# Optimization experiments

Measured on AMD Instinct MI355X. Metric: run time of the kernel, lower is better.

## Reference

```python
import jax, jax.numpy as jnp
import numpy as np

NEG_INF = -9e15
ALPHA = 2.0  # LeakyReLU negative slope from init (alpha=2)


def setup_inputs() -> dict:
    key = jax.random.key(0)
    k1, k2, k3, k4 = jax.random.split(key, 4)
    B, N, Fin, Fout = 8, 2048, 256, 128
    x = jax.random.normal(k1, (B, N, Fin), dtype=jnp.float32)
    adj = jax.random.randint(k2, (B, N, N), 0, 2, dtype=jnp.int32)
    # xavier_uniform with gain=1.414
    def xavier(k, shape, gain=1.414):
        fan_in, fan_out = shape[0], shape[1]
        bound = gain * np.sqrt(6.0 / (fan_in + fan_out))
        return jax.random.uniform(k, shape, jnp.float32, -bound, bound)
    W = xavier(k3, (Fin, Fout))
    a = xavier(k4, (2 * Fout, 1))
    return {"x": x, "adj": adj, "W": W, "a": a}


def reference(x, adj, W, a):
    # Wh: [B, N, Fout]
    Wh = jnp.matmul(x, W)
    Fout = W.shape[1]
    a1 = a[:Fout, 0]   # [Fout]
    a2 = a[Fout:, 0]   # [Fout]
    f1 = jnp.einsum('bnf,f->bn', Wh, a1)  # [B, N]
    f2 = jnp.einsum('bnf,f->bn', Wh, a2)  # [B, N]
    e = f1[:, :, None] + f2[:, None, :]   # [B, N, N]
    e = jnp.where(e >= 0, e, ALPHA * e)   # leaky relu, slope 2
    e = jnp.where(adj > 0, e, NEG_INF)
    attention = jax.nn.softmax(e, axis=2)
    # dropout: eval mode (no-op)
    h_prime = jnp.matmul(attention, Wh)   # [B, N, Fout]
    # concat=True -> elu
    return jnp.where(h_prime > 0, h_prime, jnp.expm1(h_prime))
```

## Files before the change

kernel.cpp:

```cpp
#include <hip/hip_runtime.h>
#include <hip/hip_bf16.h>
#include <math.h>

constexpr int B_   = 8;
constexpr int N_   = 2048;
constexpr int FIN  = 256;
constexpr int FOUT = 128;

constexpr int CH  = 512;
constexpr int NCH = N_ / CH;
constexpr int PR  = CH + 8;
constexpr int XR  = FIN + 8;
constexpr int TR  = 40;

typedef __attribute__((ext_vector_type(8))) short bf16x8;
typedef __attribute__((ext_vector_type(4))) float f32x4;
typedef __attribute__((ext_vector_type(4))) int   i32x4;

static __device__ __forceinline__ unsigned short f2bf(float f) {
    __hip_bfloat16 h = __float2bfloat16(f);
    return *reinterpret_cast<unsigned short*>(&h);
}
static __device__ __forceinline__ i32x4 ntload4(const int* p) {
    return __builtin_nontemporal_load((const i32x4*)p);
}

__global__ __launch_bounds__(256) void k0_wt(const float* __restrict__ W,
                                             unsigned short* __restrict__ Wt) {
    const int n = blockIdx.x;
    const int k = threadIdx.x;
    Wt[n * FIN + k] = f2bf(W[k * FOUT + n]);
}

__global__ __launch_bounds__(256) void ka_wh(const float* __restrict__ x,
                                             const unsigned short* __restrict__ Wt,
                                             const float* __restrict__ a,
                                             unsigned short* __restrict__ WhT,
                                             float* __restrict__ f1,
                                             float* __restrict__ f2) {
    __shared__ unsigned short xs[32 * XR];
    __shared__ float as[2 * FOUT];
    __shared__ float fred[2][4][32];

    const int tid = threadIdx.x;
    const int j0  = blockIdx.x * 32;
    const int b   = j0 >> 11;
    const int jb  = j0 & (N_ - 1);

    if (tid < 2 * FOUT) as[tid] = a[tid];
    {
        const float4* xsrc = (const float4*)(x + (size_t)j0 * FIN);
#pragma unroll
        for (int t = 0; t < 8; ++t) {
            const int idx = tid + t * 256;
            float4 v = xsrc[idx];
            const int row = idx >> 6, c4 = idx & 63;
            ushort4 u;
            u.x = f2bf(v.x); u.y = f2bf(v.y); u.z = f2bf(v.z); u.w = f2bf(v.w);
            *(ushort4*)&xs[row * XR + c4 * 4] = u;
        }
    }
    __syncthreads();

    const int wave = tid >> 6, lane = tid & 63;
    const int quad = lane >> 4, l16 = lane & 15;

    f32x4 acc[2][2];
#pragma unroll
    for (int aa = 0; aa < 2; ++aa)
#pragma unroll
        for (int nn = 0; nn < 2; ++nn) acc[aa][nn] = {0.f, 0.f, 0.f, 0.f};

    const unsigned short* wtA0 = Wt + (size_t)(32 * wave + l16) * FIN;
    const unsigned short* wtA1 = wtA0 + 16 * FIN;
#pragma unroll
    for (int ks = 0; ks < FIN / 32; ++ks) {
        const int kof = ks * 32 + quad * 8;
        bf16x8 af0 = *(const bf16x8*)&wtA0[kof];
        bf16x8 af1 = *(const bf16x8*)&wtA1[kof];
        bf16x8 bf0 = *(const bf16x8*)&xs[l16 * XR + kof];
        bf16x8 bf1 = *(const bf16x8*)&xs[(16 + l16) * XR + kof];
        acc[0][0] = __builtin_amdgcn_mfma_f32_16x16x32_bf16(af0, bf0, acc[0][0], 0, 0, 0);
        acc[0][1] = __builtin_amdgcn_mfma_f32_16x16x32_bf16(af0, bf1, acc[0][1], 0, 0, 0);
        acc[1][0] = __builtin_amdgcn_mfma_f32_16x16x32_bf16(af1, bf0, acc[1][0], 0, 0, 0);
        acc[1][1] = __builtin_amdgcn_mfma_f32_16x16x32_bf16(af1, bf1, acc[1][1], 0, 0, 0);
    }
    __syncthreads();

    unsigned short* T = xs;
    float pf[2][2] = {{0.f, 0.f}, {0.f, 0.f}};
#pragma unroll
    for (int aa = 0; aa < 2; ++aa)
#pragma unroll
        for (int nn = 0; nn < 2; ++nn)
#pragma unroll
            for (int r = 0; r < 4; ++r) {
                const int d = 32 * wave + 16 * aa + 4 * quad + r;
                const float v = acc[aa][nn][r];
                T[d * TR + nn * 16 + l16] = f2bf(v);
                pf[0][nn] += v * as[d];
                pf[1][nn] += v * as[FOUT + d];
            }
#pragma unroll
    for (int ff = 0; ff < 2; ++ff)
#pragma unroll
        for (int nn = 0; nn < 2; ++nn) {
            float v = pf[ff][nn];
            v += __shfl_xor(v, 16);
            v += __shfl_xor(v, 32);
            pf[ff][nn] = v;
        }
    if (quad == 0) {
#pragma unroll
        for (int ff = 0; ff < 2; ++ff)
#pragma unroll
            for (int nn = 0; nn < 2; ++nn)
                fred[ff][wave][nn * 16 + l16] = pf[ff][nn];
    }
    __syncthreads();

    unsigned short* dstW = WhT + (size_t)b * FOUT * N_;
#pragma unroll
    for (int it = 0; it < 2; ++it) {
        const int idx = it * 256 + tid;
        const int d = idx >> 2, q = idx & 3;
        bf16x8 v = *(const bf16x8*)&T[d * TR + q * 8];
        *(bf16x8*)&dstW[(size_t)d * N_ + jb + q * 8] = v;
    }
    if (tid < 64) {
        const int ff = tid >> 5, j32 = tid & 31;
        const float s = fred[ff][0][j32] + fred[ff][1][j32] +
                        fred[ff][2][j32] + fred[ff][3][j32];
        (ff ? f2 : f1)[(size_t)b * N_ + jb + j32] = s;
    }
}

__global__ __launch_bounds__(512, 4) void kb_attn(const int* __restrict__ adj,
                                                  const unsigned short* __restrict__ WhT,
                                                  const float* __restrict__ f1,
                                                  const float* __restrict__ f2,
                                                  float* __restrict__ out) {
    __shared__ unsigned short p[2][16 * PR];
    __shared__ float rsum[16];

    const int tid  = threadIdx.x;
    const int b    = blockIdx.x & 7;
    const int i0   = (blockIdx.x >> 3) * 16;
    const int wave = tid >> 6, lane = tid & 63;
    const int quad = lane >> 4, l16 = lane & 15;

    const float4* f2b4 = (const float4*)(f2 + (size_t)b * N_);
    const int*    adjB = adj + (size_t)b * N_ * N_;

    float f1r[2], s_run[2];
#pragma unroll
    for (int rr = 0; rr < 2; ++rr) {
        f1r[rr]   = f1[(size_t)b * N_ + i0 + wave * 2 + rr];
        s_run[rr] = 0.f;
    }

    f32x4 acc = {0.f, 0.f, 0.f, 0.f};
    const unsigned short* wBr =
        WhT + (size_t)b * FOUT * N_ + (size_t)(wave * 16 + l16) * N_;

    i32x4  areg[2][2];
    float4 fv[2];

    auto LOADS = [&](int c) {
        fv[0] = f2b4[c * (CH / 4) + lane];
        fv[1] = f2b4[c * (CH / 4) + 64 + lane];
#pragma unroll
        for (int rr = 0; rr < 2; ++rr) {
            const int* arow =
                adjB + (size_t)(i0 + wave * 2 + rr) * N_ + c * CH;
            areg[rr][0] = ntload4(arow + 4 * lane);
            areg[rr][1] = ntload4(arow + 256 + 4 * lane);
        }
    };

    auto PROCESS = [&](int c) {
        unsigned short* pb = &p[c & 1][0];
#pragma unroll
        for (int rr = 0; rr < 2; ++rr) {
            const int ti = wave * 2 + rr;
            const float f1i = f1r[rr];
            const i32x4 av0 = areg[rr][0];
            const i32x4 av1 = areg[rr][1];

            float e[8];
            e[0] = f1i + fv[0].x; e[1] = f1i + fv[0].y;
            e[2] = f1i + fv[0].z; e[3] = f1i + fv[0].w;
            e[4] = f1i + fv[1].x; e[5] = f1i + fv[1].y;
            e[6] = f1i + fv[1].z; e[7] = f1i + fv[1].w;
#pragma unroll
            for (int q = 0; q < 8; ++q) e[q] = (e[q] >= 0.f) ? e[q] : 2.f * e[q];

            float pv[8];
            pv[0] = (av0.x > 0) ? __expf(e[0]) : 0.f;
            pv[1] = (av0.y > 0) ? __expf(e[1]) : 0.f;
            pv[2] = (av0.z > 0) ? __expf(e[2]) : 0.f;
            pv[3] = (av0.w > 0) ? __expf(e[3]) : 0.f;
            pv[4] = (av1.x > 0) ? __expf(e[4]) : 0.f;
            pv[5] = (av1.y > 0) ? __expf(e[5]) : 0.f;
            pv[6] = (av1.z > 0) ? __expf(e[6]) : 0.f;
            pv[7] = (av1.w > 0) ? __expf(e[7]) : 0.f;

            s_run[rr] += ((pv[0] + pv[1]) + (pv[2] + pv[3])) +
                         ((pv[4] + pv[5]) + (pv[6] + pv[7]));

            ushort4 u0, u1;
            u0.x = f2bf(pv[0]); u0.y = f2bf(pv[1]);
            u0.z = f2bf(pv[2]); u0.w = f2bf(pv[3]);
            u1.x = f2bf(pv[4]); u1.y = f2bf(pv[5]);
            u1.z = f2bf(pv[6]); u1.w = f2bf(pv[7]);
            *(ushort4*)&pb[ti * PR + 4 * lane]       = u0;
            *(ushort4*)&pb[ti * PR + 256 + 4 * lane] = u1;
        }
    };

    LOADS(0);
    PROCESS(0);
    __syncthreads();

    for (int c = 0; c < NCH; ++c) {
        const unsigned short* wBc = wBr + (size_t)c * CH;
        bf16x8 br[16];
#pragma unroll
        for (int ks = 0; ks < CH / 32; ++ks)
            br[ks] = *(const bf16x8*)&wBc[ks * 32 + quad * 8];

        if (c + 1 < NCH) LOADS(c + 1);

        const unsigned short* pA = &p[c & 1][l16 * PR];
#pragma unroll
        for (int ks = 0; ks < CH / 32; ++ks) {
            bf16x8 afr = *(const bf16x8*)&pA[ks * 32 + quad * 8];
            acc = __builtin_amdgcn_mfma_f32_16x16x32_bf16(afr, br[ks], acc,
                                                          0, 0, 0);
        }

        if (c + 1 < NCH) {
            PROCESS(c + 1);
        } else {
#pragma unroll
            for (int rr = 0; rr < 2; ++rr) {
                float s = s_run[rr];
#pragma unroll
                for (int o = 32; o; o >>= 1) s += __shfl_xor(s, o);
                if (lane == 0) rsum[wave * 2 + rr] = s;
            }
        }
        __syncthreads();
    }

#pragma unroll
    for (int r = 0; r < 4; ++r) {
        const int m = quad * 4 + r;
        const float inv = 1.f / rsum[m];
        float v = acc[r] * inv;
        v = (v > 0.f) ? v : expm1f(v);
        out[((size_t)b * N_ + i0 + m) * FOUT + wave * 16 + l16] = v;
    }
}

extern "C" void kernel_launch(void* const* d_in, const int* in_sizes, int n_in,
                              void* d_out, int out_size, void* d_ws, size_t ws_size,
                              hipStream_t stream) {
    const float* x   = (const float*)d_in[0];
    const int*   adj = (const int*)d_in[1];
    const float* W   = (const float*)d_in[2];
    const float* a   = (const float*)d_in[3];
    float* out = (float*)d_out;

    unsigned short* WhT = (unsigned short*)d_ws;
    unsigned short* Wt  = WhT + (size_t)B_ * FOUT * N_;
    float* f1 = (float*)(Wt + (size_t)FOUT * FIN);
    float* f2 = f1 + (size_t)B_ * N_;

    hipLaunchKernelGGL(k0_wt, dim3(FOUT), dim3(FIN), 0, stream, W, Wt);
    hipLaunchKernelGGL(ka_wh, dim3(B_ * N_ / 32), dim3(256), 0, stream,
                       x, Wt, a, WhT, f1, f2);
    hipLaunchKernelGGL(kb_attn, dim3(B_ * N_ / 16), dim3(512), 0, stream,
                       adj, WhT, f1, f2, out);
}
```

Before: 260.2 us.

## Precompute adjacency bitmask in a separate kernel and consume bits in attention

Adds a pre-pass kernel that streams the int32 adjacency matrix once and packs it into 64-bit ballot bitmasks. The attention kernel then reads only these compact mask words instead of adjacency ints, and its chunk loop is reordered so the next chunk is processed before the current chunk's MFMA loads. The full adjacency read is still paid in the pre-pass, so total traffic does not drop. The change adds a launch and a mask write/read round trip, and removes the software prefetch that overlapped adjacency loads with MFMA work.

```diff
diff --git a/kernel.cpp b/kernel.cpp
--- a/kernel.cpp
+++ b/kernel.cpp
@@ -30,6 +30,29 @@
     const int n = blockIdx.x;
     const int k = threadIdx.x;
     Wt[n * FIN + k] = f2bf(W[k * FOUT + n]);
+}
+
+__global__ __launch_bounds__(256) void kp_mask(const int* __restrict__ adj,
+                                               unsigned long long* __restrict__ maskW) {
+    const int lane   = threadIdx.x & 63;
+    const int wid    = (blockIdx.x * 256 + threadIdx.x) >> 6;
+    const int nwaves = (2048 * 256) >> 6;
+    const int ngrp   = (B_ * N_ * N_) / 256;
+
+    for (int g = wid; g < ngrp; g += nwaves) {
+        const int* base = adj + (size_t)g * 256 + 4 * lane;
+        i32x4 v = ntload4(base);
+        unsigned long long b0 = __ballot(v[0] > 0);
+        unsigned long long b1 = __ballot(v[1] > 0);
+        unsigned long long b2 = __ballot(v[2] > 0);
+        unsigned long long b3 = __ballot(v[3] > 0);
+        if (lane < 4) {
+            unsigned long long w = (lane == 0) ? b0
+                                 : (lane == 1) ? b1
+                                 : (lane == 2) ? b2 : b3;
+            maskW[(size_t)4 * g + lane] = w;
+        }
+    }
 }
 
 __global__ __launch_bounds__(256) void ka_wh(const float* __restrict__ x,
@@ -135,7 +158,7 @@
     }
 }
 
-__global__ __launch_bounds__(512, 4) void kb_attn(const int* __restrict__ adj,
+__global__ __launch_bounds__(512, 4) void kb_attn(const unsigned long long* __restrict__ maskW,
                                                   const unsigned short* __restrict__ WhT,
                                                   const float* __restrict__ f1,
                                                   const float* __restrict__ f2,
@@ -149,8 +172,7 @@
     const int wave = tid >> 6, lane = tid & 63;
     const int quad = lane >> 4, l16 = lane & 15;
 
-    const float4* f2b4 = (const float4*)(f2 + (size_t)b * N_);
-    const int*    adjB = adj + (size_t)b * N_ * N_;
+    const f32x4* f2b4 = (const f32x4*)(f2 + (size_t)b * N_);
 
     float f1r[2], s_run[2];
 #pragma unroll
@@ -163,47 +185,39 @@
     const unsigned short* wBr =
         WhT + (size_t)b * FOUT * N_ + (size_t)(wave * 16 + l16) * N_;
 
-    i32x4  areg[2][2];
-    float4 fv[2];
-
-    auto LOADS = [&](int c) {
-        fv[0] = f2b4[c * (CH / 4) + lane];
-        fv[1] = f2b4[c * (CH / 4) + 64 + lane];
-#pragma unroll
-        for (int rr = 0; rr < 2; ++rr) {
-            const int* arow =
-                adjB + (size_t)(i0 + wave * 2 + rr) * N_ + c * CH;
-            areg[rr][0] = ntload4(arow + 4 * lane);
-            areg[rr][1] = ntload4(arow + 256 + 4 * lane);
-        }
-    };
-
     auto PROCESS = [&](int c) {
         unsigned short* pb = &p[c & 1][0];
+        const f32x4 fva = f2b4[c * (CH / 4) + lane];
+        const f32x4 fvb = f2b4[c * (CH / 4) + 64 + lane];
 #pragma unroll
         for (int rr = 0; rr < 2; ++rr) {
             const int ti = wave * 2 + rr;
             const float f1i = f1r[rr];
-            const i32x4 av0 = areg[rr][0];
-            const i32x4 av1 = areg[rr][1];
+            const size_t gbase =
+                (((size_t)b * N_ + (size_t)(i0 + ti)) * N_ + (size_t)c * CH) >> 8;
+            const unsigned long long* mw = maskW + 4 * gbase;
+            const unsigned long long m00 = mw[0], m01 = mw[1];
+            const unsigned long long m02 = mw[2], m03 = mw[3];
+            const unsigned long long m10 = mw[4], m11 = mw[5];
+            const unsigned long long m12 = mw[6], m13 = mw[7];
 
             float e[8];
-            e[0] = f1i + fv[0].x; e[1] = f1i + fv[0].y;
-            e[2] = f1i + fv[0].z; e[3] = f1i + fv[0].w;
-            e[4] = f1i + fv[1].x; e[5] = f1i + fv[1].y;
-            e[6] = f1i + fv[1].z; e[7] = f1i + fv[1].w;
+            e[0] = f1i + fva[0]; e[1] = f1i + fva[1];
+            e[2] = f1i + fva[2]; e[3] = f1i + fva[3];
+            e[4] = f1i + fvb[0]; e[5] = f1i + fvb[1];
+            e[6] = f1i + fvb[2]; e[7] = f1i + fvb[3];
 #pragma unroll
             for (int q = 0; q < 8; ++q) e[q] = (e[q] >= 0.f) ? e[q] : 2.f * e[q];
 
             float pv[8];
-            pv[0] = (av0.x > 0) ? __expf(e[0]) : 0.f;
-            pv[1] = (av0.y > 0) ? __expf(e[1]) : 0.f;
-            pv[2] = (av0.z > 0) ? __expf(e[2]) : 0.f;
-            pv[3] = (av0.w > 0) ? __expf(e[3]) : 0.f;
-            pv[4] = (av1.x > 0) ? __expf(e[4]) : 0.f;
-            pv[5] = (av1.y > 0) ? __expf(e[5]) : 0.f;
-            pv[6] = (av1.z > 0) ? __expf(e[6]) : 0.f;
-            pv[7] = (av1.w > 0) ? __expf(e[7]) : 0.f;
+            pv[0] = ((m00 >> lane) & 1ull) ? __expf(e[0]) : 0.f;
+            pv[1] = ((m01 >> lane) & 1ull) ? __expf(e[1]) : 0.f;
+            pv[2] = ((m02 >> lane) & 1ull) ? __expf(e[2]) : 0.f;
+            pv[3] = ((m03 >> lane) & 1ull) ? __expf(e[3]) : 0.f;
+            pv[4] = ((m10 >> lane) & 1ull) ? __expf(e[4]) : 0.f;
+            pv[5] = ((m11 >> lane) & 1ull) ? __expf(e[5]) : 0.f;
+            pv[6] = ((m12 >> lane) & 1ull) ? __expf(e[6]) : 0.f;
+            pv[7] = ((m13 >> lane) & 1ull) ? __expf(e[7]) : 0.f;
 
             s_run[rr] += ((pv[0] + pv[1]) + (pv[2] + pv[3])) +
                          ((pv[4] + pv[5]) + (pv[6] + pv[7]));
@@ -218,27 +232,10 @@
         }
     };
 
-    LOADS(0);
     PROCESS(0);
     __syncthreads();
 
     for (int c = 0; c < NCH; ++c) {
-        const unsigned short* wBc = wBr + (size_t)c * CH;
-        bf16x8 br[16];
-#pragma unroll
-        for (int ks = 0; ks < CH / 32; ++ks)
-            br[ks] = *(const bf16x8*)&wBc[ks * 32 + quad * 8];
-
-        if (c + 1 < NCH) LOADS(c + 1);
-
-        const unsigned short* pA = &p[c & 1][l16 * PR];
-#pragma unroll
-        for (int ks = 0; ks < CH / 32; ++ks) {
-            bf16x8 afr = *(const bf16x8*)&pA[ks * 32 + quad * 8];
-            acc = __builtin_amdgcn_mfma_f32_16x16x32_bf16(afr, br[ks], acc,
-                                                          0, 0, 0);
-        }
-
         if (c + 1 < NCH) {
             PROCESS(c + 1);
         } else {
@@ -249,6 +246,16 @@
                 for (int o = 32; o; o >>= 1) s += __shfl_xor(s, o);
                 if (lane == 0) rsum[wave * 2 + rr] = s;
             }
+        }
+
+        const unsigned short* wBc = wBr + (size_t)c * CH;
+        const unsigned short* pA = &p[c & 1][l16 * PR];
+#pragma unroll
+        for (int ks = 0; ks < CH / 32; ++ks) {
+            bf16x8 bfr = *(const bf16x8*)&wBc[ks * 32 + quad * 8];
+            bf16x8 afr = *(const bf16x8*)&pA[ks * 32 + quad * 8];
+            acc = __builtin_amdgcn_mfma_f32_16x16x32_bf16(afr, bfr, acc,
+                                                          0, 0, 0);
         }
         __syncthreads();
     }
@@ -276,10 +283,12 @@
     unsigned short* Wt  = WhT + (size_t)B_ * FOUT * N_;
     float* f1 = (float*)(Wt + (size_t)FOUT * FIN);
     float* f2 = f1 + (size_t)B_ * N_;
+    unsigned long long* maskW = (unsigned long long*)(f2 + (size_t)B_ * N_);
 
     hipLaunchKernelGGL(k0_wt, dim3(FOUT), dim3(FIN), 0, stream, W, Wt);
+    hipLaunchKernelGGL(kp_mask, dim3(2048), dim3(256), 0, stream, adj, maskW);
     hipLaunchKernelGGL(ka_wh, dim3(B_ * N_ / 32), dim3(256), 0, stream,
                        x, Wt, a, WhT, f1, f2);
     hipLaunchKernelGGL(kb_attn, dim3(B_ * N_ / 16), dim3(512), 0, stream,
-                       adj, WhT, f1, f2, out);
-}
+                       maskW, WhT, f1, f2, out);
+}
```

New measurement: 277.3 us. 1.07x slower.
